# Kernel optimization log

Measured on AMD Instinct MI355X. Metric: run time of the kernel, lower is better.

Reference implementation:

```python
import jax, jax.numpy as jnp
import numpy as np

EPS = 1e-12  # matches torch F.normalize default eps

def _l2_normalize(x):
    # torch.nn.functional.normalize: x / max(||x||_2, eps)
    n = jnp.sqrt(jnp.sum(x * x, axis=-1, keepdims=True))
    return x / jnp.maximum(n, EPS)

def setup_inputs() -> dict:
    key = jax.random.key(0)
    kq, kk, kv = jax.random.split(key, 3)
    B, N, M, C = 8, 4096, 4096, 256
    return {
        "query": jax.random.normal(kq, (B, N, C), dtype=jnp.float32),
        "key": jax.random.normal(kk, (B, M, C), dtype=jnp.float32),
        "value": jax.random.normal(kv, (B, M, C), dtype=jnp.float32),
    }

def reference(query, key, value):
    B, N, C = query.shape
    q = _l2_normalize(query)          # (B, N, C)
    k = _l2_normalize(key)            # (B, M, C)
    kv = jnp.einsum('bmc,bmd->bcd', k, value)   # (B, C, C)
    context = jnp.einsum('bnc,bcd->bnd', q, kv) # (B, N, C)
    return context / N
```

## Files before the change

### kernel.cpp

```cpp
#include <hip/hip_runtime.h>

typedef __attribute__((ext_vector_type(4))) float v4f;
typedef __attribute__((ext_vector_type(8))) short short8;
typedef unsigned short u16;
typedef unsigned int u32;
typedef __attribute__((ext_vector_type(2))) unsigned int u32x2;
typedef __attribute__((ext_vector_type(4))) unsigned short u16x4;
typedef __attribute__((ext_vector_type(8))) unsigned short u16x8;

#define CDIM 256
#define NB 8
#define NN 4096
#define MM 4096

static __device__ __forceinline__ u16 f2bf(float f) {
  unsigned u = __float_as_uint(f);
  u = (u + 0x7fffu + ((u >> 16) & 1u)) >> 16;
  return (u16)u;
}
static __device__ __forceinline__ float bf2f(u16 h) {
  return __uint_as_float(((unsigned)h) << 16);
}
static __device__ __forceinline__ u32 pack2(float a, float b) {
  return (u32)f2bf(a) | ((u32)f2bf(b) << 16);
}

static __device__ __forceinline__ int sidx32(int c, int m) {
  return (c * 32 + m) ^ (((c >> 1) & 7) << 3);
}

static __device__ __forceinline__ u32x2 xpose4(u32 A, u32 B, int hi) {
  u32 tA = (u32)__shfl_xor((int)A, 32);
  u32 tB = (u32)__shfl_xor((int)B, 32);
  u32 U = (hi < 2) ? A : tB;
  u32 V = (hi < 2) ? tA : B;
  u32 tU = (u32)__shfl_xor((int)U, 16);
  u32 tV = (u32)__shfl_xor((int)V, 16);
  u32 Up, Vp;
  if ((hi & 1) == 0) {
    Up = (U & 0xffffu) | (tU << 16);
    Vp = (V & 0xffffu) | (tV << 16);
  } else {
    Up = (tU >> 16) | (U & 0xffff0000u);
    Vp = (tV >> 16) | (V & 0xffff0000u);
  }
  return (u32x2){Up, Vp};
}

#define BARRIER() do { \
  asm volatile("s_waitcnt lgkmcnt(0)" ::: "memory"); \
  __builtin_amdgcn_s_barrier(); \
  __builtin_amdgcn_sched_barrier(0); \
} while (0)

__global__ __launch_bounds__(512) void kv_kernel(const float* __restrict__ key,
                                                 const float* __restrict__ value,
                                                 u16* __restrict__ partial, int KC) {
  __shared__ __align__(16) u16 KL[2][256 * 32];
  __shared__ __align__(16) u16 VL[2][256 * 32];
  int t = threadIdx.x;
  int b = blockIdx.y, s = blockIdx.x;
  int w = t >> 6, lane = t & 63, lo = lane & 15, hi = lane >> 4;

  const float* kbase = key + ((size_t)b * MM + (size_t)s * KC) * CDIM;
  const float* vbase = value + ((size_t)b * MM + (size_t)s * KC) * CDIM;

  v4f acc[2][16];
  #pragma unroll
  for (int i = 0; i < 2; i++)
    #pragma unroll
    for (int d = 0; d < 16; d++) acc[i][d] = (v4f){0.f, 0.f, 0.f, 0.f};

  v4f kqA[4], vqA[4], kqB[4], vqB[4];

  auto LOADS = [&](int sc, v4f (&kq)[4], v4f (&vq)[4]) {
    int row = sc * 32 + w * 4 + hi;
    const float* kr = kbase + (size_t)row * CDIM + lo * 4;
    const float* vr = vbase + (size_t)row * CDIM + lo * 4;
    #pragma unroll
    for (int qt = 0; qt < 4; ++qt) {
      kq[qt] = *(const v4f*)(kr + qt * 64);
      vq[qt] = *(const v4f*)(vr + qt * 64);
    }
  };
  auto STORE = [&](int bufi, v4f (&kq)[4], v4f (&vq)[4]) {
    int m0 = w * 4;
    float ss = 0.f;
    #pragma unroll
    for (int qt = 0; qt < 4; ++qt)
      ss += kq[qt][0]*kq[qt][0] + kq[qt][1]*kq[qt][1] + kq[qt][2]*kq[qt][2] + kq[qt][3]*kq[qt][3];
    #pragma unroll
    for (int m = 1; m < 16; m <<= 1) ss += __shfl_xor(ss, m);
    float sc_ = 1.0f / fmaxf(sqrtf(ss), 1e-12f);
    #pragma unroll
    for (int qt = 0; qt < 4; ++qt) {
      int c = qt * 64 + lo * 4 + hi;
      int idx = sidx32(c, m0);
      u32x2 ko = xpose4(pack2(kq[qt][0] * sc_, kq[qt][1] * sc_),
                        pack2(kq[qt][2] * sc_, kq[qt][3] * sc_), hi);
      *(u32x2*)&KL[bufi][idx] = ko;
      u32x2 vo = xpose4(pack2(vq[qt][0], vq[qt][1]),
                        pack2(vq[qt][2], vq[qt][3]), hi);
      *(u32x2*)&VL[bufi][idx] = vo;
    }
  };
  auto MF = [&](const u16* KB, const u16* VB) {
    int acol = hi * 8;
    int r0 = w * 32 + lo, r1 = w * 32 + 16 + lo;
    short8 a0 = *(const short8*)&KB[sidx32(r0, 0) ^ 0 ? sidx32(r0, 0) : sidx32(r0, 0)];
    a0 = *(const short8*)&KB[(r0 * 32 + acol) ^ (((r0 >> 1) & 7) << 3)];
    short8 a1 = *(const short8*)&KB[(r1 * 32 + acol) ^ (((r1 >> 1) & 7) << 3)];
    #pragma unroll
    for (int dt = 0; dt < 16; ++dt) {
      int drow = dt * 16 + lo;
      short8 bb = *(const short8*)&VB[(drow * 32 + acol) ^ (((drow >> 1) & 7) << 3)];
      acc[0][dt] = __builtin_amdgcn_mfma_f32_16x16x32_bf16(bb, a0, acc[0][dt], 0, 0, 0);
      acc[1][dt] = __builtin_amdgcn_mfma_f32_16x16x32_bf16(bb, a1, acc[1][dt], 0, 0, 0);
    }
  };

  int nsc = KC >> 5;
  LOADS(0, kqA, vqA);
  LOADS(1, kqB, vqB);
  STORE(0, kqA, vqA);
  BARRIER();
  for (int i = 0; i < nsc; i += 2) {
    if (i + 2 < nsc) LOADS(i + 2, kqA, vqA);
    MF(KL[0], VL[0]);
    if (i + 1 < nsc) {
      STORE(1, kqB, vqB);
      BARRIER();
      if (i + 3 < nsc) LOADS(i + 3, kqB, vqB);
      MF(KL[1], VL[1]);
      if (i + 2 < nsc) {
        STORE(0, kqA, vqA);
        BARRIER();
      }
    }
  }

  size_t base = ((size_t)(s * NB + b)) << 16;
  #pragma unroll
  for (int i = 0; i < 2; i++) {
    int cc = w * 32 + i * 16 + lo;
    #pragma unroll
    for (int dt = 0; dt < 16; ++dt) {
      int dd = dt * 16 + hi * 4;
      #pragma unroll
      for (int r = 0; r < 4; r++)
        partial[base + (size_t)(dd + r) * 256 + cc] = f2bf(acc[i][dt][r]);
    }
  }
}

__global__ __launch_bounds__(256) void red_kernel(const u16* __restrict__ partial,
                                                  u16* __restrict__ kvT, int splits) {
  int j = blockIdx.x * 256 + threadIdx.x;
  int b = j >> 13;
  int e0 = (j & 8191) * 8;
  size_t off = ((size_t)b << 16) + e0;
  const float inv = 1.0f / 4096.0f;
  float sum[8] = {0.f, 0.f, 0.f, 0.f, 0.f, 0.f, 0.f, 0.f};
  for (int s = 0; s < splits; ++s) {
    u16x8 p = *(const u16x8*)&partial[(((size_t)s * NB) << 16) + off];
    #pragma unroll
    for (int x = 0; x < 8; ++x) sum[x] += bf2f(p[x]);
  }
  u16x8 o;
  #pragma unroll
  for (int x = 0; x < 8; ++x) o[x] = f2bf(sum[x] * inv);
  *(u16x8*)&kvT[off] = o;
}

__global__ __launch_bounds__(512) void ctx_kernel(const float* __restrict__ query,
                                                  const u16* __restrict__ kvT,
                                                  float* __restrict__ out) {
  __shared__ __align__(16) u16 qn[2][16 * 256];
  int t = threadIdx.x;
  int b = blockIdx.y;
  int tile0 = blockIdx.x * 4;
  int w = t >> 6, lane = t & 63, lo = lane & 15, hi = lane >> 4;
  int row = t >> 5, l32 = t & 31;
  const float* qbase = query + (size_t)b * NN * CDIM + (size_t)row * CDIM + l32 * 8;

  const float* qr0 = qbase + (size_t)(tile0 * 16) * CDIM;
  v4f x0 = *(const v4f*)qr0;
  v4f x1 = *(const v4f*)(qr0 + 4);

  const u16* kvb = kvT + ((size_t)b << 16);
  short8 Bf[2][8];
  #pragma unroll
  for (int i = 0; i < 2; i++) {
    int dr = (2 * w + i) * 16 + lo;
    #pragma unroll
    for (int kc = 0; kc < 8; kc++)
      Bf[i][kc] = *(const short8*)&kvb[(size_t)dr * 256 + kc * 32 + 8 * hi];
  }

  {
    float ss = x0[0]*x0[0] + x0[1]*x0[1] + x0[2]*x0[2] + x0[3]*x0[3]
             + x1[0]*x1[0] + x1[1]*x1[1] + x1[2]*x1[2] + x1[3]*x1[3];
    #pragma unroll
    for (int m = 1; m < 32; m <<= 1) ss += __shfl_xor(ss, m);
    float sc = 1.0f / fmaxf(sqrtf(ss), 1e-12f);
    u16x8 qb;
    qb[0] = f2bf(x0[0] * sc); qb[1] = f2bf(x0[1] * sc);
    qb[2] = f2bf(x0[2] * sc); qb[3] = f2bf(x0[3] * sc);
    qb[4] = f2bf(x1[0] * sc); qb[5] = f2bf(x1[1] * sc);
    qb[6] = f2bf(x1[2] * sc); qb[7] = f2bf(x1[3] * sc);
    *(u16x8*)&qn[0][(row * 256 + l32 * 8) ^ ((row & 7) << 3)] = qb;
  }

  int cur = 0;
  #pragma unroll
  for (int nt = 0; nt < 4; ++nt) {
    v4f p0, p1;
    if (nt < 3) {
      const float* qr = qbase + (size_t)((tile0 + nt + 1) * 16) * CDIM;
      p0 = *(const v4f*)qr;
      p1 = *(const v4f*)(qr + 4);
    }
    __syncthreads();
    short8 Af[8];
    #pragma unroll
    for (int kc = 0; kc < 8; kc++)
      Af[kc] = *(const short8*)&qn[cur][(lo * 256 + kc * 32 + 8 * hi) ^ ((lo & 7) << 3)];
    v4f acc0 = (v4f){0.f, 0.f, 0.f, 0.f};
    v4f acc1 = (v4f){0.f, 0.f, 0.f, 0.f};
    #pragma unroll
    for (int kc = 0; kc < 8; kc++) {
      acc0 = __builtin_amdgcn_mfma_f32_16x16x32_bf16(Af[kc], Bf[0][kc], acc0, 0, 0, 0);
      acc1 = __builtin_amdgcn_mfma_f32_16x16x32_bf16(Af[kc], Bf[1][kc], acc1, 0, 0, 0);
    }
    int n0 = (tile0 + nt) * 16;
    #pragma unroll
    for (int r = 0; r < 4; r++) {
      size_t ro = (size_t)(b * NN + n0 + 4 * hi + r) * CDIM;
      out[ro + (2 * w) * 16 + lo] = acc0[r];
      out[ro + (2 * w + 1) * 16 + lo] = acc1[r];
    }
    if (nt < 3) {
      float ss = p0[0]*p0[0] + p0[1]*p0[1] + p0[2]*p0[2] + p0[3]*p0[3]
               + p1[0]*p1[0] + p1[1]*p1[1] + p1[2]*p1[2] + p1[3]*p1[3];
      #pragma unroll
      for (int m = 1; m < 32; m <<= 1) ss += __shfl_xor(ss, m);
      float sc = 1.0f / fmaxf(sqrtf(ss), 1e-12f);
      u16x8 qb;
      qb[0] = f2bf(p0[0] * sc); qb[1] = f2bf(p0[1] * sc);
      qb[2] = f2bf(p0[2] * sc); qb[3] = f2bf(p0[3] * sc);
      qb[4] = f2bf(p1[0] * sc); qb[5] = f2bf(p1[1] * sc);
      qb[6] = f2bf(p1[2] * sc); qb[7] = f2bf(p1[3] * sc);
      *(u16x8*)&qn[cur ^ 1][(row * 256 + l32 * 8) ^ ((row & 7) << 3)] = qb;
      cur ^= 1;
    }
  }
}

extern "C" void kernel_launch(void* const* d_in, const int* in_sizes, int n_in,
                              void* d_out, int out_size, void* d_ws, size_t ws_size,
                              hipStream_t stream) {
  const float* q = (const float*)d_in[0];
  const float* k = (const float*)d_in[1];
  const float* v = (const float*)d_in[2];
  float* out = (float*)d_out;

  int splits = 32;
  while (splits > 2) {
    size_t need = ((size_t)splits + 1ull) * 1048576ull;
    if (need <= ws_size) break;
    splits >>= 1;
  }
  u16* partial = (u16*)d_ws;
  u16* kvT = (u16*)((char*)d_ws + (size_t)splits * 1048576ull);

  kv_kernel<<<dim3(splits, NB), dim3(512), 0, stream>>>(k, v, partial, MM / splits);
  red_kernel<<<dim3(256), dim3(256), 0, stream>>>(partial, kvT, splits);
  ctx_kernel<<<dim3(64, NB), dim3(512), 0, stream>>>(q, kvT, out);
}
```

Measured before the change: 57.78 us.

## Split kv_kernel across value-column halves and coalesce partial stores

```diff
diff --git a/kernel.cpp b/kernel.cpp
--- a/kernel.cpp
+++ b/kernel.cpp
@@ -5,7 +5,7 @@
 typedef unsigned short u16;
 typedef unsigned int u32;
 typedef __attribute__((ext_vector_type(2))) unsigned int u32x2;
-typedef __attribute__((ext_vector_type(4))) unsigned short u16x4;
+typedef __attribute__((ext_vector_type(4))) unsigned int u32x4;
 typedef __attribute__((ext_vector_type(8))) unsigned short u16x8;
 
 #define CDIM 256
@@ -57,33 +57,32 @@
                                                  const float* __restrict__ value,
                                                  u16* __restrict__ partial, int KC) {
   __shared__ __align__(16) u16 KL[2][256 * 32];
-  __shared__ __align__(16) u16 VL[2][256 * 32];
+  __shared__ __align__(16) u16 VL[2][128 * 32];
   int t = threadIdx.x;
-  int b = blockIdx.y, s = blockIdx.x;
+  int b = blockIdx.y, s = blockIdx.x, h = blockIdx.z;
   int w = t >> 6, lane = t & 63, lo = lane & 15, hi = lane >> 4;
 
   const float* kbase = key + ((size_t)b * MM + (size_t)s * KC) * CDIM;
-  const float* vbase = value + ((size_t)b * MM + (size_t)s * KC) * CDIM;
-
-  v4f acc[2][16];
+  const float* vbase = value + ((size_t)b * MM + (size_t)s * KC) * CDIM + h * 128;
+
+  v4f acc[2][8];
   #pragma unroll
   for (int i = 0; i < 2; i++)
     #pragma unroll
-    for (int d = 0; d < 16; d++) acc[i][d] = (v4f){0.f, 0.f, 0.f, 0.f};
-
-  v4f kqA[4], vqA[4], kqB[4], vqB[4];
-
-  auto LOADS = [&](int sc, v4f (&kq)[4], v4f (&vq)[4]) {
+    for (int d = 0; d < 8; d++) acc[i][d] = (v4f){0.f, 0.f, 0.f, 0.f};
+
+  v4f kqA[4], vqA[2], kqB[4], vqB[2];
+
+  auto LOADS = [&](int sc, v4f (&kq)[4], v4f (&vq)[2]) {
     int row = sc * 32 + w * 4 + hi;
     const float* kr = kbase + (size_t)row * CDIM + lo * 4;
     const float* vr = vbase + (size_t)row * CDIM + lo * 4;
     #pragma unroll
-    for (int qt = 0; qt < 4; ++qt) {
-      kq[qt] = *(const v4f*)(kr + qt * 64);
-      vq[qt] = *(const v4f*)(vr + qt * 64);
-    }
+    for (int qt = 0; qt < 4; ++qt) kq[qt] = *(const v4f*)(kr + qt * 64);
+    #pragma unroll
+    for (int qt = 0; qt < 2; ++qt) vq[qt] = *(const v4f*)(vr + qt * 64);
   };
-  auto STORE = [&](int bufi, v4f (&kq)[4], v4f (&vq)[4]) {
+  auto STORE = [&](int bufi, v4f (&kq)[4], v4f (&vq)[2]) {
     int m0 = w * 4;
     float ss = 0.f;
     #pragma unroll
@@ -95,23 +94,25 @@
     #pragma unroll
     for (int qt = 0; qt < 4; ++qt) {
       int c = qt * 64 + lo * 4 + hi;
-      int idx = sidx32(c, m0);
       u32x2 ko = xpose4(pack2(kq[qt][0] * sc_, kq[qt][1] * sc_),
                         pack2(kq[qt][2] * sc_, kq[qt][3] * sc_), hi);
-      *(u32x2*)&KL[bufi][idx] = ko;
+      *(u32x2*)&KL[bufi][sidx32(c, m0)] = ko;
+    }
+    #pragma unroll
+    for (int qt = 0; qt < 2; ++qt) {
+      int c = qt * 64 + lo * 4 + hi;
       u32x2 vo = xpose4(pack2(vq[qt][0], vq[qt][1]),
                         pack2(vq[qt][2], vq[qt][3]), hi);
-      *(u32x2*)&VL[bufi][idx] = vo;
+      *(u32x2*)&VL[bufi][sidx32(c, m0)] = vo;
     }
   };
   auto MF = [&](const u16* KB, const u16* VB) {
     int acol = hi * 8;
     int r0 = w * 32 + lo, r1 = w * 32 + 16 + lo;
-    short8 a0 = *(const short8*)&KB[sidx32(r0, 0) ^ 0 ? sidx32(r0, 0) : sidx32(r0, 0)];
-    a0 = *(const short8*)&KB[(r0 * 32 + acol) ^ (((r0 >> 1) & 7) << 3)];
+    short8 a0 = *(const short8*)&KB[(r0 * 32 + acol) ^ (((r0 >> 1) & 7) << 3)];
     short8 a1 = *(const short8*)&KB[(r1 * 32 + acol) ^ (((r1 >> 1) & 7) << 3)];
     #pragma unroll
-    for (int dt = 0; dt < 16; ++dt) {
+    for (int dt = 0; dt < 8; ++dt) {
       int drow = dt * 16 + lo;
       short8 bb = *(const short8*)&VB[(drow * 32 + acol) ^ (((drow >> 1) & 7) << 3)];
       acc[0][dt] = __builtin_amdgcn_mfma_f32_16x16x32_bf16(bb, a0, acc[0][dt], 0, 0, 0);
@@ -139,37 +140,47 @@
     }
   }
 
-  size_t base = ((size_t)(s * NB + b)) << 16;
-  #pragma unroll
-  for (int i = 0; i < 2; i++) {
-    int cc = w * 32 + i * 16 + lo;
-    #pragma unroll
-    for (int dt = 0; dt < 16; ++dt) {
-      int dd = dt * 16 + hi * 4;
+  u32* p32 = (u32*)partial;
+  size_t sbase = (((size_t)(s * NB + b)) * 2 + h) * 16384;
+  #pragma unroll
+  for (int i = 0; i < 2; i++)
+    #pragma unroll
+    for (int dt = 0; dt < 8; ++dt)
       #pragma unroll
-      for (int r = 0; r < 4; r++)
-        partial[base + (size_t)(dd + r) * 256 + cc] = f2bf(acc[i][dt][r]);
-    }
-  }
+      for (int p = 0; p < 2; ++p) {
+        int reg32 = i * 16 + dt * 2 + p;
+        p32[sbase + reg32 * 512 + t] = pack2(acc[i][dt][2 * p], acc[i][dt][2 * p + 1]);
+      }
 }
 
 __global__ __launch_bounds__(256) void red_kernel(const u16* __restrict__ partial,
                                                   u16* __restrict__ kvT, int splits) {
+  const u32* p32 = (const u32*)partial;
   int j = blockIdx.x * 256 + threadIdx.x;
   int b = j >> 13;
-  int e0 = (j & 8191) * 8;
-  size_t off = ((size_t)b << 16) + e0;
+  int F = (j & 8191) * 4;
+  int h = F >> 14, reg32 = (F >> 9) & 31, T0 = F & 511;
+  int i = reg32 >> 4, dt = (reg32 >> 1) & 7, p = reg32 & 1;
   const float inv = 1.0f / 4096.0f;
   float sum[8] = {0.f, 0.f, 0.f, 0.f, 0.f, 0.f, 0.f, 0.f};
-  for (int s = 0; s < splits; ++s) {
-    u16x8 p = *(const u16x8*)&partial[(((size_t)s * NB) << 16) + off];
-    #pragma unroll
-    for (int x = 0; x < 8; ++x) sum[x] += bf2f(p[x]);
-  }
-  u16x8 o;
-  #pragma unroll
-  for (int x = 0; x < 8; ++x) o[x] = f2bf(sum[x] * inv);
-  *(u16x8*)&kvT[off] = o;
+  size_t off = (size_t)h * 16384 + (size_t)reg32 * 512 + T0;
+  for (int s2 = 0; s2 < splits; ++s2) {
+    u32x4 v = *(const u32x4*)&p32[((size_t)(s2 * NB + b)) * 32768 + off];
+    #pragma unroll
+    for (int x = 0; x < 4; ++x) {
+      sum[2 * x]     += bf2f((u16)(v[x] & 0xffffu));
+      sum[2 * x + 1] += bf2f((u16)(v[x] >> 16));
+    }
+  }
+  #pragma unroll
+  for (int tt = 0; tt < 4; ++tt) {
+    int T = T0 + tt;
+    int w = T >> 6, lane2 = T & 63, lo = lane2 & 15, hi2 = lane2 >> 4;
+    int c = w * 32 + i * 16 + lo;
+    int d = h * 128 + dt * 16 + hi2 * 4 + 2 * p;
+    kvT[((size_t)(b * 256 + d)) * 256 + c]     = f2bf(sum[2 * tt] * inv);
+    kvT[((size_t)(b * 256 + d + 1)) * 256 + c] = f2bf(sum[2 * tt + 1] * inv);
+  }
 }
 
 __global__ __launch_bounds__(512) void ctx_kernel(const float* __restrict__ query,
@@ -273,7 +284,7 @@
   u16* partial = (u16*)d_ws;
   u16* kvT = (u16*)((char*)d_ws + (size_t)splits * 1048576ull);
 
-  kv_kernel<<<dim3(splits, NB), dim3(512), 0, stream>>>(k, v, partial, MM / splits);
+  kv_kernel<<<dim3(splits, NB, 2), dim3(512), 0, stream>>>(k, v, partial, MM / splits);
   red_kernel<<<dim3(256), dim3(256), 0, stream>>>(partial, kvT, splits);
   ctx_kernel<<<dim3(64, NB), dim3(512), 0, stream>>>(q, kvT, out);
 }
```

After: 60.60 us. 4.9% more time.
